# Kernel optimization log

Measured on AMD Instinct MI355X. Metric: run time of the kernel, lower is better.

The kernel has to match this reference:

```python
import jax, jax.numpy as jnp
import numpy as np

B, IN, OUT, G = 64, 8192, 8192, 64
NG = IN // G  # groups per row


def setup_inputs() -> dict:
    key = jax.random.key(0)
    k1, k2, k3, k4 = jax.random.split(key, 4)
    x = jax.random.normal(k1, (B, IN), dtype=jnp.float32)
    # packed 2-bit codes: 4 codes per byte, LSB-first (matches _pack2)
    w_packed = jax.random.randint(k2, (OUT, IN // 4), 0, 256, dtype=jnp.int32).astype(jnp.uint8)
    # scales from _calc_group_qparams are positive (max_abs/1.5); zp is always 2
    scales = jax.random.uniform(k3, (OUT, NG), dtype=jnp.float32, minval=0.01, maxval=0.1)
    zps = jnp.full((OUT, NG), 2, dtype=jnp.int32)
    bias = jax.random.normal(k4, (OUT,), dtype=jnp.float32) * 0.01
    return {"x": x, "w_packed": w_packed, "scales": scales, "zps": zps, "bias": bias}


def _dequant(w_packed, scales, zps):
    # unpack: byte -> 4 two-bit codes, LSB first (matches _unpack2)
    out_f = w_packed.shape[0]
    codes = jnp.stack([(w_packed >> s) & 3 for s in (0, 2, 4, 6)], axis=-1)  # [OUT, IN//4, 4]
    q = codes.reshape(out_f, NG, G).astype(jnp.int32)                        # [OUT, NG, G]
    # per-group dequant: (q - zp) * scale
    w = (q - zps[:, :, None]).astype(jnp.float32) * scales[:, :, None]
    return w.reshape(out_f, IN)                                              # [OUT, IN]


def reference(x, w_packed, scales, zps, bias):
    w = _dequant(w_packed, scales, zps)  # [OUT, IN] fp32
    # original accumulates xg @ wg.T per group; equivalent to full x @ w.T
    return x @ w.T + bias                # [B, OUT]
```

## Files before the change

### kernel.cpp

```cpp
#include <hip/hip_runtime.h>
#include <hip/hip_bf16.h>

#define B_    64
#define IN_   8192
#define OUT_  8192
#define NG_   128
#define PB_   2048

#define KSPLIT 8
#define KC     1024
#define CGS    2

typedef float f32x4 __attribute__((ext_vector_type(4)));
typedef short s16x8 __attribute__((ext_vector_type(8)));
union FU { float f; unsigned u; };

__global__ __launch_bounds__(256, 2) void k_main(
    const float* __restrict__ x,
    const unsigned char* __restrict__ wp,
    const float* __restrict__ scales,
    const int* __restrict__ zps,
    float* __restrict__ part)
{
    __shared__ uint4 x_lds[4096];

    const int tid  = threadIdx.x;
    const int wave = tid >> 6;
    const int lane = tid & 63;
    const int q    = lane >> 4;
    const int nn   = lane & 15;

    const int bid     = blockIdx.x;
    const int kidx    = bid & (KSPLIT - 1);
    const int nblk    = bid >> 3;
    const int kbase   = kidx * KC;
    const int colbase = nblk * 128 + wave * 32;

    const unsigned d0 = ((const unsigned*)wp)[0];
    const unsigned d1 = ((const unsigned*)wp)[1];
    const bool u8mode = (d0 | d1) > 255u;
    const bool zgen   = (zps[0] != 2) || (zps[OUT_ * NG_ - 1] != 2);

    uint4 w16[2][2][CGS];
    const int wb = (kbase >> 2) + q * 16;
#pragma unroll
    for (int ph = 0; ph < 2; ++ph)
#pragma unroll
        for (int sb = 0; sb < 2; ++sb)
#pragma unroll
            for (int cg = 0; cg < CGS; ++cg) {
                int n = colbase + cg * 16 + nn;
                w16[ph][sb][cg] =
                    *(const uint4*)(wp + n * PB_ + wb + ph * 128 + sb * 64);
            }

    auto stage = [&](int kph) {
#pragma unroll
        for (int i = 0; i < 16; ++i) {
            const float* src = x + (wave * 16 + nn) * IN_ + kph + i * 32 + q * 8;
            float4 f0 = *(const float4*)src;
            float4 f1 = *(const float4*)(src + 4);
            __hip_bfloat162 h0 = __float22bfloat162_rn(make_float2(f0.x, f0.y));
            __hip_bfloat162 h1 = __float22bfloat162_rn(make_float2(f0.z, f0.w));
            __hip_bfloat162 h2 = __float22bfloat162_rn(make_float2(f1.x, f1.y));
            __hip_bfloat162 h3 = __float22bfloat162_rn(make_float2(f1.z, f1.w));
            uint4 o;
            o.x = *(unsigned*)&h0; o.y = *(unsigned*)&h1;
            o.z = *(unsigned*)&h2; o.w = *(unsigned*)&h3;
            int val = i * 32 + q * 8;
            int sb  = val >> 8;
            int qp  = (val >> 6) & 3;
            int b   = (val >> 3) & 7;
            int sg  = sb * 32 + b * 4 + wave;
            int l   = qp * 16 + nn;
            x_lds[sg * 64 + l] = o;
        }
    };
    stage(kbase);

    if (!u8mode) {
        const int* wpi = (const int*)wp;
#pragma unroll
        for (int ph = 0; ph < 2; ++ph)
#pragma unroll
            for (int sb = 0; sb < 2; ++sb)
#pragma unroll
                for (int cg = 0; cg < CGS; ++cg) {
                    int n = colbase + cg * 16 + nn;
                    const int* p = wpi + n * PB_ + wb + ph * 128 + sb * 64;
                    uint4 a  = *(const uint4*)p;
                    uint4 b2 = *(const uint4*)(p + 4);
                    uint4 c  = *(const uint4*)(p + 8);
                    uint4 d  = *(const uint4*)(p + 12);
                    w16[ph][sb][cg].x = __builtin_amdgcn_perm(a.y,  a.x,  0x0C0C0400) |
                                        __builtin_amdgcn_perm(a.w,  a.z,  0x04000C0C);
                    w16[ph][sb][cg].y = __builtin_amdgcn_perm(b2.y, b2.x, 0x0C0C0400) |
                                        __builtin_amdgcn_perm(b2.w, b2.z, 0x04000C0C);
                    w16[ph][sb][cg].z = __builtin_amdgcn_perm(c.y,  c.x,  0x0C0C0400) |
                                        __builtin_amdgcn_perm(c.w,  c.z,  0x04000C0C);
                    w16[ph][sb][cg].w = __builtin_amdgcn_perm(d.y,  d.x,  0x0C0C0400) |
                                        __builtin_amdgcn_perm(d.w,  d.z,  0x04000C0C);
                }
    }

    float sf[2][2][CGS], fb[2][2][CGS];
#pragma unroll
    for (int ph = 0; ph < 2; ++ph)
#pragma unroll
        for (int sb = 0; sb < 2; ++sb)
#pragma unroll
            for (int cg = 0; cg < CGS; ++cg) {
                int n = colbase + cg * 16 + nn;
                int g = kidx * 16 + ph * 8 + sb * 4 + q;
                float s = scales[n * NG_ + g] * 1.001953125f;
                float zpf = zgen ? (float)zps[n * NG_ + g] : 2.0f;
                sf[ph][sb][cg] = s;
                fb[ph][sb][cg] = -zpf * s;
            }

    f32x4 acc[CGS][4];
#pragma unroll
    for (int cg = 0; cg < CGS; ++cg)
#pragma unroll
        for (int mt = 0; mt < 4; ++mt)
            acc[cg][mt] = (f32x4){0.f, 0.f, 0.f, 0.f};

    __syncthreads();

#pragma unroll
    for (int ph = 0; ph < 2; ++ph) {
        if (ph) {
            __syncthreads();
            stage(kbase + 512);
            __syncthreads();
        }
#pragma unroll
        for (int sb = 0; sb < 2; ++sb) {
#pragma unroll
            for (int d = 0; d < 4; ++d) {
#pragma unroll
                for (int h = 0; h < 2; ++h) {
                    const int b = d * 2 + h;
                    union { uint4 u4; s16x8 s8; } av[4];
#pragma unroll
                    for (int mt = 0; mt < 4; ++mt)
                        av[mt].u4 = x_lds[(sb * 32 + b * 4 + mt) * 64 + lane];
#pragma unroll
                    for (int cg = 0; cg < CGS; ++cg) {
                        const uint4 W = w16[ph][sb][cg];
                        const unsigned v = (d == 0) ? W.x : (d == 1) ? W.y
                                         : (d == 2) ? W.z : W.w;
                        const float s = sf[ph][sb][cg], fbv = fb[ph][sb][cg];
                        union { unsigned u[4]; s16x8 s8; } bf;
#pragma unroll
                        for (int m = 0; m < 4; ++m) {
                            const int sh = h * 16 + m * 4;
                            FU f0, f1;
                            f0.f = fmaf((float)((v >> sh) & 3u), s, fbv);
                            f1.f = fmaf((float)((v >> (sh + 2)) & 3u), s, fbv);
                            bf.u[m] = __builtin_amdgcn_perm(f1.u, f0.u, 0x07060302);
                        }
#pragma unroll
                        for (int mt = 0; mt < 4; ++mt)
                            acc[cg][mt] = __builtin_amdgcn_mfma_f32_16x16x32_bf16(
                                av[mt].s8, bf.s8, acc[cg][mt], 0, 0, 0);
                    }
                }
            }
        }
    }

    __syncthreads();
    float* lf = (float*)x_lds;
#pragma unroll
    for (int cg = 0; cg < CGS; ++cg)
#pragma unroll
        for (int mt = 0; mt < 4; ++mt)
#pragma unroll
            for (int r = 0; r < 4; ++r)
                lf[(mt * 16 + q * 4 + r) * 128 + wave * 32 + cg * 16 + nn] =
                    acc[cg][mt][r];
    __syncthreads();
    float* pp = part + kidx * (B_ * OUT_);
    const float4* ls = (const float4*)x_lds;
#pragma unroll
    for (int u = 0; u < 8; ++u) {
        int idx = u * 256 + tid;
        int row = idx >> 5;
        int cq  = idx & 31;
        float4 v = ls[idx];
        *(float4*)(pp + row * OUT_ + nblk * 128 + cq * 4) = v;
    }
}

__global__ __launch_bounds__(256) void k_reduce(const float* __restrict__ part,
                                                const float* __restrict__ bias,
                                                float* __restrict__ out) {
    int i = (blockIdx.x * 256 + threadIdx.x) * 4;
    float4 s = *(const float4*)(bias + (i & (OUT_ - 1)));
#pragma unroll
    for (int p = 0; p < KSPLIT; ++p) {
        float4 v = *(const float4*)(part + p * (B_ * OUT_) + i);
        s.x += v.x; s.y += v.y; s.z += v.z; s.w += v.w;
    }
    *(float4*)(out + i) = s;
}

extern "C" void kernel_launch(void* const* d_in, const int* in_sizes, int n_in,
                              void* d_out, int out_size, void* d_ws, size_t ws_size,
                              hipStream_t stream) {
    const float*         x      = (const float*)d_in[0];
    const unsigned char* wp     = (const unsigned char*)d_in[1];
    const float*         scales = (const float*)d_in[2];
    const int*           zps    = (const int*)d_in[3];
    const float*         bias   = (const float*)d_in[4];
    float*               out    = (float*)d_out;

    float* part = (float*)d_ws;

    k_main<<<512, 256, 0, stream>>>(x, wp, scales, zps, part);
    k_reduce<<<512, 256, 0, stream>>>(part, bias, out);
}
```

Baseline: 131.1 us.

## Fuse split-K reduction into main kernel via per-block completion flags

```diff
diff --git a/kernel.cpp b/kernel.cpp
--- a/kernel.cpp
+++ b/kernel.cpp
@@ -15,11 +15,18 @@
 typedef short s16x8 __attribute__((ext_vector_type(8)));
 union FU { float f; unsigned u; };
 
+__device__ __forceinline__ unsigned long long sig(int bid) {
+    unsigned hi = 0xAB000000u | (unsigned)bid;
+    return ((unsigned long long)hi << 32) | (hi ^ 0xFFFF00FFu);
+}
+
 __global__ __launch_bounds__(256, 2) void k_main(
     const float* __restrict__ x,
     const unsigned char* __restrict__ wp,
     const float* __restrict__ scales,
     const int* __restrict__ zps,
+    const float* __restrict__ bias,
+    float* __restrict__ out,
     float* __restrict__ part)
 {
     __shared__ uint4 x_lds[4096];
@@ -112,11 +119,28 @@
             for (int cg = 0; cg < CGS; ++cg) {
                 int n = colbase + cg * 16 + nn;
                 int g = kidx * 16 + ph * 8 + sb * 4 + q;
-                float s = scales[n * NG_ + g] * 1.001953125f;
-                float zpf = zgen ? (float)zps[n * NG_ + g] : 2.0f;
-                sf[ph][sb][cg] = s;
-                fb[ph][sb][cg] = -zpf * s;
-            }
+                sf[ph][sb][cg] = scales[n * NG_ + g] * 1.001953125f;
+            }
+    if (zgen) {
+#pragma unroll
+        for (int ph = 0; ph < 2; ++ph)
+#pragma unroll
+            for (int sb = 0; sb < 2; ++sb)
+#pragma unroll
+                for (int cg = 0; cg < CGS; ++cg) {
+                    int n = colbase + cg * 16 + nn;
+                    int g = kidx * 16 + ph * 8 + sb * 4 + q;
+                    fb[ph][sb][cg] = -(float)zps[n * NG_ + g] * sf[ph][sb][cg];
+                }
+    } else {
+#pragma unroll
+        for (int ph = 0; ph < 2; ++ph)
+#pragma unroll
+            for (int sb = 0; sb < 2; ++sb)
+#pragma unroll
+                for (int cg = 0; cg < CGS; ++cg)
+                    fb[ph][sb][cg] = -2.0f * sf[ph][sb][cg];
+    }
 
     f32x4 acc[CGS][4];
 #pragma unroll
@@ -181,29 +205,50 @@
                 lf[(mt * 16 + q * 4 + r) * 128 + wave * 32 + cg * 16 + nn] =
                     acc[cg][mt][r];
     __syncthreads();
-    float* pp = part + kidx * (B_ * OUT_);
+
+    unsigned long long* flags =
+        (unsigned long long*)(part + KSPLIT * (B_ * OUT_));
     const float4* ls = (const float4*)x_lds;
-#pragma unroll
-    for (int u = 0; u < 8; ++u) {
-        int idx = u * 256 + tid;
-        int row = idx >> 5;
-        int cq  = idx & 31;
-        float4 v = ls[idx];
-        *(float4*)(pp + row * OUT_ + nblk * 128 + cq * 4) = v;
-    }
-}
-
-__global__ __launch_bounds__(256) void k_reduce(const float* __restrict__ part,
-                                                const float* __restrict__ bias,
-                                                float* __restrict__ out) {
-    int i = (blockIdx.x * 256 + threadIdx.x) * 4;
-    float4 s = *(const float4*)(bias + (i & (OUT_ - 1)));
-#pragma unroll
-    for (int p = 0; p < KSPLIT; ++p) {
-        float4 v = *(const float4*)(part + p * (B_ * OUT_) + i);
-        s.x += v.x; s.y += v.y; s.z += v.z; s.w += v.w;
-    }
-    *(float4*)(out + i) = s;
+
+    if (kidx != KSPLIT - 1) {
+        float* pp = part + kidx * (B_ * OUT_);
+#pragma unroll
+        for (int u = 0; u < 8; ++u) {
+            int idx = u * 256 + tid;
+            int row = idx >> 5;
+            int cq  = idx & 31;
+            *(float4*)(pp + row * OUT_ + nblk * 128 + cq * 4) = ls[idx];
+        }
+        __threadfence();
+        __syncthreads();
+        if (tid == 0)
+            atomicExch(&flags[bid], sig(bid));
+    } else {
+        if (tid < KSPLIT - 1) {
+            int sib = nblk * KSPLIT + tid;
+            unsigned long long m = sig(sib);
+            while (atomicAdd(&flags[sib], 0ull) != m)
+                __builtin_amdgcn_s_sleep(1);
+        }
+        __syncthreads();
+        __threadfence();
+#pragma unroll
+        for (int u = 0; u < 8; ++u) {
+            int idx = u * 256 + tid;
+            int row = idx >> 5;
+            int cq  = idx & 31;
+            int off = row * OUT_ + nblk * 128 + cq * 4;
+            float4 s = *(const float4*)(bias + nblk * 128 + cq * 4);
+            float4 v = ls[idx];
+            s.x += v.x; s.y += v.y; s.z += v.z; s.w += v.w;
+#pragma unroll
+            for (int p = 0; p < KSPLIT - 1; ++p) {
+                float4 w = *(const float4*)(part + p * (B_ * OUT_) + off);
+                s.x += w.x; s.y += w.y; s.z += w.z; s.w += w.w;
+            }
+            *(float4*)(out + off) = s;
+        }
+    }
 }
 
 extern "C" void kernel_launch(void* const* d_in, const int* in_sizes, int n_in,
@@ -218,6 +263,5 @@
 
     float* part = (float*)d_ws;
 
-    k_main<<<512, 256, 0, stream>>>(x, wp, scales, zps, part);
-    k_reduce<<<512, 256, 0, stream>>>(part, bias, out);
+    k_main<<<512, 256, 0, stream>>>(x, wp, scales, zps, bias, out, part);
 }
```

New measurement: 210.5 us. +60.6%, slower.
